# Performance work log

Hardware: AMD Instinct MI355X
Metric: run time of the kernel (lower is better)

The kernel has to match this reference:

```python
import jax, jax.numpy as jnp
import numpy as np

NA = 50000   # nodes of type 'a'
NB = 50000   # nodes of type 'b'
E = 800000   # edges per cross relation
D = 256      # input feature dim == hidden_dim (SAGEConv lazy in-dim)
H = 256      # hidden_dim
EMB = 128    # embedding_dim
L = 2        # num_layer
# relation order in stacked weights: 0=(a,to,b), 1=(b,to,a), 2=(a,self_loop,a), 3=(b,self_loop,b)


def setup_inputs() -> dict:
    key = jax.random.key(0)
    ks = jax.random.split(key, 8)
    x_a = jax.random.normal(ks[0], (NA, D), jnp.float32)
    x_b = jax.random.normal(ks[1], (NB, D), jnp.float32)
    edge_ab = jax.random.randint(ks[2], (2, E), 0, NA, dtype=jnp.int32)  # row0: src in a, row1: dst in b
    edge_ba = jax.random.randint(ks[3], (2, E), 0, NB, dtype=jnp.int32)  # row0: src in b, row1: dst in a
    s = 1.0 / np.sqrt(H)
    Wl = jax.random.normal(ks[4], (L, 4, H, H), jnp.float32) * s  # lin_l weight (on aggregated neighbors)
    bl = jnp.zeros((L, 4, H), jnp.float32)                         # lin_l bias
    Wr = jax.random.normal(ks[5], (L, 4, H, H), jnp.float32) * s  # lin_r weight (root/self), no bias
    lin_W = jax.random.normal(ks[6], (H, EMB), jnp.float32) * s
    lin_b = jnp.zeros((EMB,), jnp.float32)
    return dict(x_a=x_a, x_b=x_b, edge_ab=edge_ab, edge_ba=edge_ba,
                Wl=Wl, bl=bl, Wr=Wr, lin_W=lin_W, lin_b=lin_b)


def _sage(x_src, x_dst, src, dst, n_dst, Wl, bl, Wr):
    # SAGEConv: mean-aggregate neighbor features, then lin_l(agg) + lin_r(x_dst)
    agg = jax.ops.segment_sum(x_src[src], dst, num_segments=n_dst)           # [n_dst, H]
    cnt = jax.ops.segment_sum(jnp.ones(src.shape, x_src.dtype), dst, num_segments=n_dst)
    mean = agg / jnp.maximum(cnt, 1.0)[:, None]                               # isolated dst -> 0
    return mean @ Wl + bl + x_dst @ Wr


def _sage_self(x, Wl, bl, Wr):
    # self-loop relation: each node has exactly one neighbor (itself), mean == x
    return x @ Wl + bl + x @ Wr


def reference(x_a, x_b, edge_ab, edge_ba, Wl, bl, Wr, lin_W, lin_b):
    xa, xb = x_a, x_b
    for l in range(L):
        new_a = (_sage(xb, xa, edge_ba[0], edge_ba[1], xa.shape[0], Wl[l, 1], bl[l, 1], Wr[l, 1])
                 + _sage_self(xa, Wl[l, 2], bl[l, 2], Wr[l, 2]))
        new_b = (_sage(xa, xb, edge_ab[0], edge_ab[1], xb.shape[0], Wl[l, 0], bl[l, 0], Wr[l, 0])
                 + _sage_self(xb, Wl[l, 3], bl[l, 3], Wr[l, 3]))
        xa, xb = jax.nn.relu(new_a), jax.nn.relu(new_b)
    return xa @ lin_W + lin_b, xb @ lin_W + lin_b
```

## Files before the change

### kernel.cpp

```cpp
#include <hip/hip_runtime.h>
#include <hip/hip_bf16.h>

#define NNA 50000
#define NNB 50000
#define NE  800000
#define HD  256
#define EMBD 128

typedef __attribute__((ext_vector_type(4))) int            i32x4;
typedef __attribute__((ext_vector_type(4))) float          f32x4;
typedef __attribute__((ext_vector_type(8))) short          bf16x8;
typedef __attribute__((ext_vector_type(4))) unsigned short u16x4;

static __device__ __forceinline__ float bf2f(unsigned short u) {
  union { unsigned int i; float f; } v; v.i = ((unsigned int)u) << 16; return v.f;
}
static __device__ __forceinline__ unsigned short f2bf(float f) {
  __hip_bfloat16 h = __float2bfloat16(f);
  return *reinterpret_cast<unsigned short*>(&h);
}


__global__ void k_prep_wcat(const float* __restrict__ Wl, const float* __restrict__ Wr,
                            unsigned short* __restrict__ WcatT) {
  int id = blockIdx.x * 256 + threadIdx.x;
  if (id >= 2 * 2 * 512 * 256) return;
  int n = id & 255;
  int k = (id >> 8) & 511;
  int t = (id >> 17) & 1;
  int l = id >> 18;
  int rn = (t == 0) ? 1 : 0;
  int rs = (t == 0) ? 2 : 3;
  float v;
  if (k < HD) {
    v = Wl[((l * 4 + rn) * HD + k) * HD + n];
  } else {
    int kk = k - HD;
    v = Wr[((l * 4 + rn) * HD + kk) * HD + n]
      + Wl[((l * 4 + rs) * HD + kk) * HD + n]
      + Wr[((l * 4 + rs) * HD + kk) * HD + n];
  }
  WcatT[((l * 2 + t) * HD + n) * 512 + k] = f2bf(v);
}

__global__ void k_prep_bias(const float* __restrict__ bl, float* __restrict__ bias) {
  int id = blockIdx.x * 256 + threadIdx.x;
  if (id >= 2 * 2 * 256) return;
  int n = id & 255; int t = (id >> 8) & 1; int l = id >> 9;
  int rn = (t == 0) ? 1 : 0;
  int rs = (t == 0) ? 2 : 3;
  bias[id] = bl[(l * 4 + rn) * HD + n] + bl[(l * 4 + rs) * HD + n];
}

__global__ void k_prep_lin(const float* __restrict__ linW, unsigned short* __restrict__ linWT) {
  int id = blockIdx.x * 256 + threadIdx.x;
  if (id >= EMBD * HD) return;
  int k = id & 255; int n = id >> 8;
  linWT[n * HD + k] = f2bf(linW[k * EMBD + n]);
}

__global__ void k_f32_to_bf16(const float* __restrict__ in, unsigned short* __restrict__ out, int n4) {
  int i = blockIdx.x * blockDim.x + threadIdx.x;
  int stride = gridDim.x * blockDim.x;
  for (; i < n4; i += stride) {
    f32x4 v = reinterpret_cast<const f32x4*>(in)[i];
    u16x4 o;
    o[0] = f2bf(v[0]); o[1] = f2bf(v[1]); o[2] = f2bf(v[2]); o[3] = f2bf(v[3]);
    reinterpret_cast<u16x4*>(out)[i] = o;
  }
}


__global__ void k_fill_slots(const int* __restrict__ edges, int* __restrict__ cnt,
                             int* __restrict__ slots, int nE) {
  int e = blockIdx.x * 256 + threadIdx.x;
  if (e >= nE) return;
  int src = edges[e];
  int dst = edges[nE + e];
  int pos = atomicAdd(&cnt[dst], 1);
  if (pos < 64) slots[dst * 64 + pos] = src;
}

__global__ void k_aggregate(const unsigned short* __restrict__ xsrc,
                            const int* __restrict__ slots, const int* __restrict__ cnt,
                            unsigned short* __restrict__ mean_out, int ndst) {
  int w = blockIdx.x * 4 + (threadIdx.x >> 6);
  int lane = threadIdx.x & 63;
  if (w >= ndst) return;
  int deg = cnt[w];
  int m = deg < 64 ? deg : 64;
  const int* sl = slots + w * 64;
  float a0 = 0.f, a1 = 0.f, a2 = 0.f, a3 = 0.f;
  float b0 = 0.f, b1 = 0.f, b2 = 0.f, b3 = 0.f;
  int j = 0;
  for (; j + 2 <= m; j += 2) {
    int s0 = sl[j], s1 = sl[j + 1];
    u16x4 u0 = *reinterpret_cast<const u16x4*>(xsrc + s0 * HD + lane * 4);
    u16x4 u1 = *reinterpret_cast<const u16x4*>(xsrc + s1 * HD + lane * 4);
    a0 += bf2f(u0[0]); a1 += bf2f(u0[1]); a2 += bf2f(u0[2]); a3 += bf2f(u0[3]);
    b0 += bf2f(u1[0]); b1 += bf2f(u1[1]); b2 += bf2f(u1[2]); b3 += bf2f(u1[3]);
  }
  if (j < m) {
    int s0 = sl[j];
    u16x4 u0 = *reinterpret_cast<const u16x4*>(xsrc + s0 * HD + lane * 4);
    a0 += bf2f(u0[0]); a1 += bf2f(u0[1]); a2 += bf2f(u0[2]); a3 += bf2f(u0[3]);
  }
  float inv = deg > 0 ? 1.0f / (float)deg : 0.0f;
  u16x4 o;
  o[0] = f2bf((a0 + b0) * inv);
  o[1] = f2bf((a1 + b1) * inv);
  o[2] = f2bf((a2 + b2) * inv);
  o[3] = f2bf((a3 + b3) * inv);
  *reinterpret_cast<u16x4*>(mean_out + w * HD + lane * 4) = o;
}

template <bool RELU, bool OUTF32>
__global__ __launch_bounds__(256)
void k_gemm(const unsigned short* __restrict__ Alo,
            const unsigned short* __restrict__ Ahi,
            const unsigned short* __restrict__ BT,
            const float* __restrict__ bias,
            void* __restrict__ Cout,
            int M, int N, int Ktot, int Klo) {
  __shared__ char smem[32768];
  const int t = threadIdx.x;
  const int bm = blockIdx.x, bn = blockIdx.y;
  const int lane = t & 63, wid = t >> 6;
  const int wm = wid >> 1, wn = wid & 1;
  const int l15 = lane & 15, l4 = lane >> 4;
  const int rowA0 = t >> 3;
  const int seg = t & 7;

  f32x4 acc[4][4];
#pragma unroll
  for (int i = 0; i < 4; ++i)
#pragma unroll
    for (int j = 0; j < 4; ++j) acc[i][j] = (f32x4){0.f, 0.f, 0.f, 0.f};

  const int nks = Ktot >> 6;
  for (int ks = 0; ks < nks; ++ks) {
    const int kglob = ks << 6;
    const unsigned short* Asrc = (kglob < Klo) ? Alo : Ahi;
    const int kbase = (kglob < Klo) ? kglob : (kglob - Klo);
    i32x4 ra[4], rb[4];
#pragma unroll
    for (int p = 0; p < 4; ++p) {
      int row = rowA0 + p * 32;
      int rg = bm * 128 + row;
      if (rg < M)
        ra[p] = *reinterpret_cast<const i32x4*>(Asrc + rg * HD + kbase + seg * 8);
      else
        ra[p] = (i32x4){0, 0, 0, 0};
      int ng = bn * 128 + row;
      rb[p] = *reinterpret_cast<const i32x4*>(BT + ng * Ktot + kglob + seg * 8);
    }
    __syncthreads();
#pragma unroll
    for (int p = 0; p < 4; ++p) {
      int row = rowA0 + p * 32;
      int off = row * 128 + ((seg * 16) ^ ((row & 7) << 4));
      *reinterpret_cast<i32x4*>(smem + off) = ra[p];
      *reinterpret_cast<i32x4*>(smem + 16384 + off) = rb[p];
    }
    __syncthreads();
#pragma unroll
    for (int kk = 0; kk < 2; ++kk) {
      bf16x8 af[4], bfr[4];
#pragma unroll
      for (int f = 0; f < 4; ++f) {
        int r = wm * 64 + f * 16 + l15;
        af[f] = *reinterpret_cast<const bf16x8*>(
            smem + r * 128 + ((kk * 64 + l4 * 16) ^ ((r & 7) << 4)));
        int n = wn * 64 + f * 16 + l15;
        bfr[f] = *reinterpret_cast<const bf16x8*>(
            smem + 16384 + n * 128 + ((kk * 64 + l4 * 16) ^ ((n & 7) << 4)));
      }
#pragma unroll
      for (int fm = 0; fm < 4; ++fm)
#pragma unroll
        for (int fn = 0; fn < 4; ++fn)
          acc[fm][fn] = __builtin_amdgcn_mfma_f32_16x16x32_bf16(af[fm], bfr[fn], acc[fm][fn], 0, 0, 0);
    }
  }

#pragma unroll
  for (int fm = 0; fm < 4; ++fm) {
    int row0 = bm * 128 + wm * 64 + fm * 16 + l4 * 4;
#pragma unroll
    for (int fn = 0; fn < 4; ++fn) {
      int col = bn * 128 + wn * 64 + fn * 16 + l15;
      float bv = bias[col];
      f32x4 d = acc[fm][fn];
#pragma unroll
      for (int r = 0; r < 4; ++r) {
        int rg = row0 + r;
        if (rg < M) {
          float v = d[r] + bv;
          if (RELU) v = v > 0.f ? v : 0.f;
          if (OUTF32)
            reinterpret_cast<float*>(Cout)[rg * N + col] = v;
          else
            reinterpret_cast<unsigned short*>(Cout)[rg * N + col] = f2bf(v);
        }
      }
    }
  }
}


extern "C" void kernel_launch(void* const* d_in, const int* in_sizes, int n_in,
                              void* d_out, int out_size, void* d_ws, size_t ws_size,
                              hipStream_t stream) {
  const float* x_a  = (const float*)d_in[0];
  const float* x_b  = (const float*)d_in[1];
  const int*   e_ab = (const int*)d_in[2];
  const int*   e_ba = (const int*)d_in[3];
  const float* Wl   = (const float*)d_in[4];
  const float* bl   = (const float*)d_in[5];
  const float* Wr   = (const float*)d_in[6];
  const float* linW = (const float*)d_in[7];
  const float* linb = (const float*)d_in[8];
  float* out = (float*)d_out;

  char* ws = (char*)d_ws;
  size_t off = 0;
  auto alloc = [&](size_t bytes) {
    char* p = ws + off;
    off += (bytes + 255) & ~(size_t)255;
    return p;
  };
  unsigned short* xa0    = (unsigned short*)alloc((size_t)NNA * HD * 2);
  unsigned short* xb0    = (unsigned short*)alloc((size_t)NNB * HD * 2);
  unsigned short* xa1    = (unsigned short*)alloc((size_t)NNA * HD * 2);
  unsigned short* xb1    = (unsigned short*)alloc((size_t)NNB * HD * 2);
  unsigned short* mean_a = (unsigned short*)alloc((size_t)NNA * HD * 2);
  unsigned short* mean_b = (unsigned short*)alloc((size_t)NNB * HD * 2);
  int* slots_a = (int*)alloc((size_t)NNA * 64 * 4);
  int* slots_b = (int*)alloc((size_t)NNB * 64 * 4);
  int* cnt_a   = (int*)alloc((size_t)NNA * 4);
  int* cnt_b   = (int*)alloc((size_t)NNB * 4);
  unsigned short* wcatT  = (unsigned short*)alloc((size_t)2 * 2 * 256 * 512 * 2);
  float*          biasv  = (float*)alloc((size_t)2 * 2 * 256 * 4);
  unsigned short* linWT  = (unsigned short*)alloc((size_t)EMBD * HD * 2);
  (void)ws_size; (void)in_sizes; (void)n_in; (void)out_size;

  hipMemsetAsync(cnt_a, 0, (size_t)NNA * 4, stream);
  hipMemsetAsync(cnt_b, 0, (size_t)NNB * 4, stream);

  k_prep_wcat<<<2048, 256, 0, stream>>>(Wl, Wr, wcatT);
  k_prep_bias<<<4, 256, 0, stream>>>(bl, biasv);
  k_prep_lin<<<128, 256, 0, stream>>>(linW, linWT);

  k_f32_to_bf16<<<2048, 256, 0, stream>>>(x_a, xa0, NNA * HD / 4);
  k_f32_to_bf16<<<2048, 256, 0, stream>>>(x_b, xb0, NNB * HD / 4);

  k_fill_slots<<<(NE + 255) / 256, 256, 0, stream>>>(e_ba, cnt_a, slots_a, NE);
  k_fill_slots<<<(NE + 255) / 256, 256, 0, stream>>>(e_ab, cnt_b, slots_b, NE);

  unsigned short* xa_cur = xa0; unsigned short* xb_cur = xb0;
  unsigned short* xa_nxt = xa1; unsigned short* xb_nxt = xb1;

  for (int l = 0; l < 2; ++l) {
    k_aggregate<<<NNA / 4, 256, 0, stream>>>(xb_cur, slots_a, cnt_a, mean_a, NNA);
    k_aggregate<<<NNB / 4, 256, 0, stream>>>(xa_cur, slots_b, cnt_b, mean_b, NNB);
    dim3 g((NNA + 127) / 128, 2);
    k_gemm<true, false><<<g, 256, 0, stream>>>(
        mean_a, xa_cur, wcatT + (size_t)(l * 2 + 0) * 256 * 512,
        biasv + (l * 2 + 0) * 256, xa_nxt, NNA, 256, 512, 256);
    k_gemm<true, false><<<g, 256, 0, stream>>>(
        mean_b, xb_cur, wcatT + (size_t)(l * 2 + 1) * 256 * 512,
        biasv + (l * 2 + 1) * 256, xb_nxt, NNB, 256, 512, 256);
    unsigned short* ta = xa_cur; xa_cur = xa_nxt; xa_nxt = ta;
    unsigned short* tb = xb_cur; xb_cur = xb_nxt; xb_nxt = tb;
  }

  dim3 gf((NNA + 127) / 128, 1);
  k_gemm<false, true><<<gf, 256, 0, stream>>>(
      xa_cur, xa_cur, linWT, linb, out, NNA, EMBD, 256, 256);
  k_gemm<false, true><<<gf, 256, 0, stream>>>(
      xb_cur, xb_cur, linWT, linb, out + (size_t)NNA * EMBD, NNB, EMBD, 256, 256);
}
```

Measured before the change: 554.7 us.

## Merge per-type aggregate and GEMM launches, widen gather loads with shuffled slot indices

Features and means for both node types now sit in contiguous buffers, so one aggregate launch covers both node types and each GEMM covers both types through a z-indexed batch with per-z pointer strides. The aggregation loads slot indices once per wave and broadcasts them with shuffles. Each half-wave reads 16-byte vectors from a different neighbor row, and the two halves are combined at the end with a cross-lane xor. The intent is fewer kernel launches, better tail utilization, and more memory-level parallelism in the gather, at the cost of extra shuffle instructions and index arithmetic widened to 64-bit.

```diff
diff --git a/kernel.cpp b/kernel.cpp
--- a/kernel.cpp
+++ b/kernel.cpp
@@ -11,6 +11,7 @@
 typedef __attribute__((ext_vector_type(4))) float          f32x4;
 typedef __attribute__((ext_vector_type(8))) short          bf16x8;
 typedef __attribute__((ext_vector_type(4))) unsigned short u16x4;
+typedef __attribute__((ext_vector_type(8))) unsigned short u16x8;
 
 static __device__ __forceinline__ float bf2f(unsigned short u) {
   union { unsigned int i; float f; } v; v.i = ((unsigned int)u) << 16; return v.f;
@@ -81,37 +82,72 @@
   if (pos < 64) slots[dst * 64 + pos] = src;
 }
 
-__global__ void k_aggregate(const unsigned short* __restrict__ xsrc,
-                            const int* __restrict__ slots, const int* __restrict__ cnt,
-                            unsigned short* __restrict__ mean_out, int ndst) {
+__global__ __launch_bounds__(256)
+void k_aggregate(const unsigned short* __restrict__ xa,
+                 const unsigned short* __restrict__ xb,
+                 const int* __restrict__ slots_a, const int* __restrict__ cnt_a,
+                 const int* __restrict__ slots_b, const int* __restrict__ cnt_b,
+                 unsigned short* __restrict__ mean_a, unsigned short* __restrict__ mean_b) {
   int w = blockIdx.x * 4 + (threadIdx.x >> 6);
   int lane = threadIdx.x & 63;
-  if (w >= ndst) return;
-  int deg = cnt[w];
+  const unsigned short* xsrc;
+  const int* sl;
+  int deg;
+  unsigned short* outp;
+  if (w < NNA) {
+    xsrc = xb; sl = slots_a + (size_t)w * 64; deg = cnt_a[w];
+    outp = mean_a + (size_t)w * HD;
+  } else {
+    int v = w - NNA;
+    xsrc = xa; sl = slots_b + (size_t)v * 64; deg = cnt_b[v];
+    outp = mean_b + (size_t)v * HD;
+  }
   int m = deg < 64 ? deg : 64;
-  const int* sl = slots + w * 64;
-  float a0 = 0.f, a1 = 0.f, a2 = 0.f, a3 = 0.f;
-  float b0 = 0.f, b1 = 0.f, b2 = 0.f, b3 = 0.f;
+  int s_all = sl[lane];
+  const int half = lane >> 5;
+  const int l31 = lane & 31;
+
+  float acc[8];
+#pragma unroll
+  for (int k = 0; k < 8; ++k) acc[k] = 0.f;
+
   int j = 0;
+  for (; j + 8 <= m; j += 8) {
+    int sj[4];
+#pragma unroll
+    for (int i = 0; i < 4; ++i) sj[i] = __shfl(s_all, j + 2 * i + half);
+    u16x8 v[4];
+#pragma unroll
+    for (int i = 0; i < 4; ++i)
+      v[i] = *reinterpret_cast<const u16x8*>(xsrc + (size_t)sj[i] * HD + l31 * 8);
+#pragma unroll
+    for (int i = 0; i < 4; ++i)
+#pragma unroll
+      for (int k = 0; k < 8; ++k) acc[k] += bf2f(v[i][k]);
+  }
   for (; j + 2 <= m; j += 2) {
-    int s0 = sl[j], s1 = sl[j + 1];
-    u16x4 u0 = *reinterpret_cast<const u16x4*>(xsrc + s0 * HD + lane * 4);
-    u16x4 u1 = *reinterpret_cast<const u16x4*>(xsrc + s1 * HD + lane * 4);
-    a0 += bf2f(u0[0]); a1 += bf2f(u0[1]); a2 += bf2f(u0[2]); a3 += bf2f(u0[3]);
-    b0 += bf2f(u1[0]); b1 += bf2f(u1[1]); b2 += bf2f(u1[2]); b3 += bf2f(u1[3]);
-  }
-  if (j < m) {
-    int s0 = sl[j];
-    u16x4 u0 = *reinterpret_cast<const u16x4*>(xsrc + s0 * HD + lane * 4);
-    a0 += bf2f(u0[0]); a1 += bf2f(u0[1]); a2 += bf2f(u0[2]); a3 += bf2f(u0[3]);
-  }
+    int sj = __shfl(s_all, j + half);
+    u16x8 v = *reinterpret_cast<const u16x8*>(xsrc + (size_t)sj * HD + l31 * 8);
+#pragma unroll
+    for (int k = 0; k < 8; ++k) acc[k] += bf2f(v[k]);
+  }
+  if (j < m && half == 0) {
+    int sj = __shfl(s_all, j);
+    u16x8 v = *reinterpret_cast<const u16x8*>(xsrc + (size_t)sj * HD + l31 * 8);
+#pragma unroll
+    for (int k = 0; k < 8; ++k) acc[k] += bf2f(v[k]);
+  }
+
+#pragma unroll
+  for (int k = 0; k < 8; ++k) acc[k] += __shfl_xor(acc[k], 32);
+
   float inv = deg > 0 ? 1.0f / (float)deg : 0.0f;
-  u16x4 o;
-  o[0] = f2bf((a0 + b0) * inv);
-  o[1] = f2bf((a1 + b1) * inv);
-  o[2] = f2bf((a2 + b2) * inv);
-  o[3] = f2bf((a3 + b3) * inv);
-  *reinterpret_cast<u16x4*>(mean_out + w * HD + lane * 4) = o;
+  if (half == 0) {
+    u16x8 o;
+#pragma unroll
+    for (int k = 0; k < 8; ++k) o[k] = f2bf(acc[k] * inv);
+    *reinterpret_cast<u16x8*>(outp + l31 * 8) = o;
+  }
 }
 
 template <bool RELU, bool OUTF32>
@@ -121,7 +157,15 @@
             const unsigned short* __restrict__ BT,
             const float* __restrict__ bias,
             void* __restrict__ Cout,
-            int M, int N, int Ktot, int Klo) {
+            int M, int N, int Ktot, int Klo,
+            long long sA, long long sB, long long sBias, long long sCbytes) {
+  const int z = blockIdx.z;
+  Alo += (long long)z * sA;
+  Ahi += (long long)z * sA;
+  BT += (long long)z * sB;
+  bias += (long long)z * sBias;
+  Cout = (void*)((char*)Cout + (long long)z * sCbytes);
+
   __shared__ char smem[32768];
   const int t = threadIdx.x;
   const int bm = blockIdx.x, bn = blockIdx.y;
@@ -148,11 +192,11 @@
       int row = rowA0 + p * 32;
       int rg = bm * 128 + row;
       if (rg < M)
-        ra[p] = *reinterpret_cast<const i32x4*>(Asrc + rg * HD + kbase + seg * 8);
+        ra[p] = *reinterpret_cast<const i32x4*>(Asrc + (size_t)rg * HD + kbase + seg * 8);
       else
         ra[p] = (i32x4){0, 0, 0, 0};
       int ng = bn * 128 + row;
-      rb[p] = *reinterpret_cast<const i32x4*>(BT + ng * Ktot + kglob + seg * 8);
+      rb[p] = *reinterpret_cast<const i32x4*>(BT + (size_t)ng * Ktot + kglob + seg * 8);
     }
     __syncthreads();
 #pragma unroll
@@ -198,9 +242,9 @@
           float v = d[r] + bv;
           if (RELU) v = v > 0.f ? v : 0.f;
           if (OUTF32)
-            reinterpret_cast<float*>(Cout)[rg * N + col] = v;
+            reinterpret_cast<float*>(Cout)[(size_t)rg * N + col] = v;
           else
-            reinterpret_cast<unsigned short*>(Cout)[rg * N + col] = f2bf(v);
+            reinterpret_cast<unsigned short*>(Cout)[(size_t)rg * N + col] = f2bf(v);
         }
       }
     }
@@ -229,12 +273,9 @@
     off += (bytes + 255) & ~(size_t)255;
     return p;
   };
-  unsigned short* xa0    = (unsigned short*)alloc((size_t)NNA * HD * 2);
-  unsigned short* xb0    = (unsigned short*)alloc((size_t)NNB * HD * 2);
-  unsigned short* xa1    = (unsigned short*)alloc((size_t)NNA * HD * 2);
-  unsigned short* xb1    = (unsigned short*)alloc((size_t)NNB * HD * 2);
-  unsigned short* mean_a = (unsigned short*)alloc((size_t)NNA * HD * 2);
-  unsigned short* mean_b = (unsigned short*)alloc((size_t)NNB * HD * 2);
+  unsigned short* x0   = (unsigned short*)alloc((size_t)2 * NNA * HD * 2);
+  unsigned short* x1   = (unsigned short*)alloc((size_t)2 * NNA * HD * 2);
+  unsigned short* mean = (unsigned short*)alloc((size_t)2 * NNA * HD * 2);
   int* slots_a = (int*)alloc((size_t)NNA * 64 * 4);
   int* slots_b = (int*)alloc((size_t)NNB * 64 * 4);
   int* cnt_a   = (int*)alloc((size_t)NNA * 4);
@@ -251,32 +292,30 @@
   k_prep_bias<<<4, 256, 0, stream>>>(bl, biasv);
   k_prep_lin<<<128, 256, 0, stream>>>(linW, linWT);
 
-  k_f32_to_bf16<<<2048, 256, 0, stream>>>(x_a, xa0, NNA * HD / 4);
-  k_f32_to_bf16<<<2048, 256, 0, stream>>>(x_b, xb0, NNB * HD / 4);
+  k_f32_to_bf16<<<2048, 256, 0, stream>>>(x_a, x0, NNA * HD / 4);
+  k_f32_to_bf16<<<2048, 256, 0, stream>>>(x_b, x0 + (size_t)NNA * HD, NNB * HD / 4);
 
   k_fill_slots<<<(NE + 255) / 256, 256, 0, stream>>>(e_ba, cnt_a, slots_a, NE);
   k_fill_slots<<<(NE + 255) / 256, 256, 0, stream>>>(e_ab, cnt_b, slots_b, NE);
 
-  unsigned short* xa_cur = xa0; unsigned short* xb_cur = xb0;
-  unsigned short* xa_nxt = xa1; unsigned short* xb_nxt = xb1;
+  unsigned short* xcur = x0;
+  unsigned short* xnxt = x1;
 
   for (int l = 0; l < 2; ++l) {
-    k_aggregate<<<NNA / 4, 256, 0, stream>>>(xb_cur, slots_a, cnt_a, mean_a, NNA);
-    k_aggregate<<<NNB / 4, 256, 0, stream>>>(xa_cur, slots_b, cnt_b, mean_b, NNB);
-    dim3 g((NNA + 127) / 128, 2);
+    k_aggregate<<<(NNA + NNB) / 4, 256, 0, stream>>>(
+        xcur, xcur + (size_t)NNA * HD, slots_a, cnt_a, slots_b, cnt_b,
+        mean, mean + (size_t)NNA * HD);
+    dim3 g((NNA + 127) / 128, 2, 2);
     k_gemm<true, false><<<g, 256, 0, stream>>>(
-        mean_a, xa_cur, wcatT + (size_t)(l * 2 + 0) * 256 * 512,
-        biasv + (l * 2 + 0) * 256, xa_nxt, NNA, 256, 512, 256);
-    k_gemm<true, false><<<g, 256, 0, stream>>>(
-        mean_b, xb_cur, wcatT + (size_t)(l * 2 + 1) * 256 * 512,
-        biasv + (l * 2 + 1) * 256, xb_nxt, NNB, 256, 512, 256);
-    unsigned short* ta = xa_cur; xa_cur = xa_nxt; xa_nxt = ta;
-    unsigned short* tb = xb_cur; xb_cur = xb_nxt; xb_nxt = tb;
-  }
-
-  dim3 gf((NNA + 127) / 128, 1);
+        mean, xcur, wcatT + (size_t)l * 2 * 256 * 512, biasv + l * 2 * 256, xnxt,
+        NNA, 256, 512, 256,
+        (long long)NNA * HD, 256 * 512, 256, (long long)NNA * HD * 2);
+    unsigned short* tmp = xcur; xcur = xnxt; xnxt = tmp;
+  }
+
+  dim3 gf((NNA + 127) / 128, 1, 2);
   k_gemm<false, true><<<gf, 256, 0, stream>>>(
-      xa_cur, xa_cur, linWT, linb, out, NNA, EMBD, 256, 256);
-  k_gemm<false, true><<<gf, 256, 0, stream>>>(
-      xb_cur, xb_cur, linWT, linb, out + (size_t)NNA * EMBD, NNB, EMBD, 256, 256);
-}
+      xcur, xcur, linWT, linb, out,
+      NNA, EMBD, 256, 256,
+      (long long)NNA * HD, 0, 0, (long long)NNA * EMBD * 4);
+}
```

Result: faster. 503.7 us (-9.2%).
